# Performance work log

Hardware: AMD Instinct MI355X
Metric: run time of the kernel (lower is better)

The kernel has to match this reference:

```python
import jax, jax.numpy as jnp
import numpy as np

C = 3                     # num_classes
HNM_RATIO = 3
W_OBJ = W_CLS = W_LOC = 1.0
IOU_POS, IOU_NEG = 0.5, 0.4
B, M = 32, 16
SCALES = [(160, 160), (80, 80), (40, 40)]
SIZES = [0.08, 0.16, 0.28]     # A square anchor sizes per grid cell
A = len(SIZES)


def _grid_anchors(H, W):
    # anchors ordered as ((h*W + w)*A + a), matching the permute/reshape of predictions
    cy = (np.arange(H, dtype=np.float32) + 0.5) / H
    cx = (np.arange(W, dtype=np.float32) + 0.5) / W
    cyg, cxg = np.meshgrid(cy, cx, indexing='ij')                 # [H,W]
    cyg = np.broadcast_to(cyg[..., None], (H, W, A))
    cxg = np.broadcast_to(cxg[..., None], (H, W, A))
    sz = np.broadcast_to(np.asarray(SIZES, np.float32), (H, W, A))
    anc = np.stack([cxg, cyg, sz, sz], axis=-1).reshape(-1, 4)     # [H*W*A,4] cxcywh
    return jnp.asarray(anc)


def _corners(b):  # cxcywh -> x1y1x2y2
    return jnp.concatenate([b[..., :2] - b[..., 2:] / 2, b[..., :2] + b[..., 2:] / 2], axis=-1)


def _iou(a, b):  # a [N,4], b [M,4] in corner format -> [N,M]
    lt = jnp.maximum(a[:, None, :2], b[None, :, :2])
    rb = jnp.minimum(a[:, None, 2:], b[None, :, 2:])
    wh = jnp.clip(rb - lt, 0.0)
    inter = wh[..., 0] * wh[..., 1]
    aa = (a[:, 2] - a[:, 0]) * (a[:, 3] - a[:, 1])
    ab = (b[:, 2] - b[:, 0]) * (b[:, 3] - b[:, 1])
    return inter / (aa[:, None] + ab[None, :] - inter + 1e-9)


def _loss_one(P, boxes, labels, anc):
    # P: [A*(5+C), H, W]; boxes: [M,4] cxcywh; labels: [M] int; anc: [N,4] cxcywh
    Ch, H, Wd = P.shape
    N = H * Wd * A
    P = P.transpose(1, 2, 0).reshape(N, 5 + C)
    loc, obj, cls = P[:, :4], P[:, 4], P[:, 5:]
    # --- anchor matching ---
    iou = _iou(_corners(anc), _corners(boxes))            # [N,M]
    best = iou.max(axis=1)
    midx = iou.argmax(axis=1)
    pos = best >= IOU_POS
    neg = best < IOU_NEG
    mlab = labels[midx]                                   # [N]
    mbox = boxes[midx]                                    # [N,4]
    # --- objectness BCE with hard negative mining ---
    obj_t = pos.astype(obj.dtype)
    obj_all = jnp.maximum(obj, 0) - obj * obj_t + jnp.log1p(jnp.exp(-jnp.abs(obj)))
    obj_d = jax.lax.stop_gradient(obj_all)
    npos = pos.sum()
    avail = neg.sum()
    k = jnp.where(npos == 0, jnp.minimum(100, avail), jnp.minimum(HNM_RATIO * npos, avail))
    s = jnp.sort(jnp.where(neg, obj_d, -jnp.inf))[::-1]   # descending neg losses
    thr = s[jnp.clip(k - 1, 0, N - 1)]
    sel = jnp.where(k > 0, neg & (obj_d >= thr), neg)
    mask = pos | sel
    cnt = mask.sum()
    l_obj = jnp.where(cnt > 0, (obj_all * mask).sum() / jnp.maximum(cnt, 1), 0.0)
    # --- classification CE over positives ---
    logp = jax.nn.log_softmax(cls, axis=-1)
    cls_t = jnp.clip(mlab - 1, 0, C - 1)
    ce = -jnp.take_along_axis(logp, cls_t[:, None], axis=1)[:, 0]
    l_cls = jnp.where(npos > 0, (ce * pos).sum() / jnp.maximum(npos, 1), 0.0)
    # --- localization SmoothL1 over positives ---
    t = jnp.concatenate([(mbox[:, :2] - anc[:, :2]) / anc[:, 2:],
                         jnp.log(mbox[:, 2:] / anc[:, 2:])], axis=1)
    d = jnp.abs(loc - t)
    sl1 = jnp.where(d < 1.0, 0.5 * d * d, d - 0.5)
    l_loc = jnp.where(npos > 0, (sl1 * pos[:, None]).sum() / (jnp.maximum(npos, 1) * 4), 0.0)
    return l_obj, l_cls, l_loc


def setup_inputs() -> dict:
    key = jax.random.key(0)
    ks = jax.random.split(key, 7)
    preds = [jax.random.normal(ks[i], (B, A * (5 + C), H, W), dtype=jnp.float32)
             for i, (H, W) in enumerate(SCALES)]
    ancs = [_grid_anchors(H, W) for (H, W) in SCALES]
    cxy = jax.random.uniform(ks[3], (B, M, 2), minval=0.1, maxval=0.9)
    wh = jax.random.uniform(ks[4], (B, M, 2), minval=0.05, maxval=0.3)
    boxes = jnp.concatenate([cxy, wh], axis=-1).astype(jnp.float32)   # cxcywh
    labels = jax.random.randint(ks[5], (B, M), 1, C + 1, dtype=jnp.int32)
    return {"pred0": preds[0], "pred1": preds[1], "pred2": preds[2],
            "anc0": ancs[0], "anc1": ancs[1], "anc2": ancs[2],
            "boxes": boxes, "labels": labels}


def reference(pred0, pred1, pred2, anc0, anc1, anc2, boxes, labels):
    lo = lc = ll = 0.0
    for P, anc in ((pred0, anc0), (pred1, anc1), (pred2, anc2)):
        o, c, l = jax.vmap(_loss_one, in_axes=(0, 0, 0, None))(P, boxes, labels, anc)
        lo = lo + o.sum(); lc = lc + c.sum(); ll = ll + l.sum()
    Bn = pred0.shape[0]
    loss_obj, loss_cls, loss_loc = lo / Bn, lc / Bn, ll / Bn
    loss_total = W_OBJ * loss_obj + W_CLS * loss_cls + W_LOC * loss_loc
    return jnp.stack([loss_obj, loss_cls, loss_loc, loss_total])
```

## Files before the change

### kernel.cpp

```cpp
#include <hip/hip_runtime.h>
#include <math.h>

#define ANUM 3
#define CNUM 3
#define BNUM 32
#define MNUM 16
#define CH 24
#define NBIN 4096
#define NSEG 96
#define CAP 8192
#define CHUNK 4800
#define CPB 21

__device__ __align__(16) int   g_hist[NSEG*NBIN];
__device__ __align__(16) float g_cand[(size_t)NSEG*CAP];
__device__ int   g_ccnt[NSEG];
__device__ int   g_T[NSEG];
__device__ int   g_kk[NSEG];
__device__ int   g_cab[NSEG];
__device__ float g_sab[NSEG];
__device__ float g_acc[NSEG*5];
__device__ float g_lsum[3];
__device__ int   g_done;

__device__ __forceinline__ float wred(float v){
  #pragma unroll
  for (int off=32; off; off>>=1) v += __shfl_down(v, off, 64);
  return v;
}
__device__ __forceinline__ int wredi(int v){
  #pragma unroll
  for (int off=32; off; off>>=1) v += __shfl_down(v, off, 64);
  return v;
}

__device__ __forceinline__ void seg_map(int c, int& s, int& ci){
  if (c < 16){ s = 0; ci = c; }
  else if (c < 20){ s = 1; ci = c - 16; }
  else { s = 2; ci = 0; }
}
__device__ __forceinline__ void seg_geom(int s, int& N, size_t& segbase){
  N = (s==0) ? 76800 : ((s==1) ? 19200 : 4800);
  segbase = (s==0) ? 0
          : ((s==1) ? (size_t)BNUM*76800
                    : (size_t)BNUM*(76800+19200));
}

__global__ __launch_bounds__(256) void kinit(){
  const int gid = blockIdx.x*256 + threadIdx.x;
  ((int4*)g_hist)[gid] = make_int4(0,0,0,0);
  if (gid < NSEG*5) g_acc[gid] = 0.f;
  if (gid < 3) g_lsum[gid] = 0.f;
  if (gid == 3) g_done = 0;
  if (gid < NSEG){ g_ccnt[gid]=0; g_sab[gid]=0.f; }
}

template<int H, int W, int SCALE>
__device__ __forceinline__ void k1_work(
    const float* __restrict__ pred, float* __restrict__ negvals,
    const float* sbox, const int* slab, int b, int pix, int* lh, float* f)
{
  constexpr int HW = H*W;
  constexpr int N = HW*ANUM;
  constexpr size_t segbase = (SCALE==0) ? 0
                           : ((SCALE==1) ? (size_t)BNUM*76800
                                         : (size_t)BNUM*(76800+19200));
  const bool valid = (pix < HW);
  const int pp = valid ? pix : 0;
  const int h = pp / W, w = pp % W;
  const float cx = ((float)w + 0.5f)/(float)W;
  const float cy = ((float)h + 0.5f)/(float)H;

  const float* pb = pred + (size_t)b*CH*HW;
  float obj[3];
  #pragma unroll
  for (int a=0;a<3;a++) obj[a] = pb[(a*8+4)*HW + pp];

  float ax0[3],ay0[3],ax1[3],ay1[3],areaA[3];
  #pragma unroll
  for (int a=0;a<3;a++){
    const float sz=(a==0)?0.08f:((a==1)?0.16f:0.28f);
    const float hs=sz*0.5f;
    ax0[a]=cx-hs; ay0[a]=cy-hs; ax1[a]=cx+hs; ay1[a]=cy+hs;
    areaA[a]=(ax1[a]-ax0[a])*(ay1[a]-ay0[a]);
  }
  float bi[3]={-1.f,-1.f,-1.f}, bu[3]={1.f,1.f,1.f};
  int bm[3]={0,0,0};
  #pragma unroll
  for (int m=0;m<MNUM;m++){
    const float bcx=sbox[4*m], bcy=sbox[4*m+1], bw=sbox[4*m+2], bh=sbox[4*m+3];
    const float bx0=bcx-bw*0.5f, by0=bcy-bh*0.5f, bx1=bcx+bw*0.5f, by1=bcy+bh*0.5f;
    const float areaB=(bx1-bx0)*(by1-by0);
    #pragma unroll
    for (int a=0;a<3;a++){
      float iw=fminf(ax1[a],bx1)-fmaxf(ax0[a],bx0);
      float ih=fminf(ay1[a],by1)-fmaxf(ay0[a],by0);
      iw=fmaxf(iw,0.f); ih=fmaxf(ih,0.f);
      const float inter=iw*ih;
      const float uni=areaA[a]+areaB-inter+1e-9f;
      if (inter*bu[a] > bi[a]*uni){ bi[a]=inter; bu[a]=uni; bm[a]=m; }
    }
  }
  #pragma unroll
  for (int a=0;a<3;a++){
    const float best = bi[a]/bu[a];
    const bool pos = best >= 0.5f;
    const bool neg = best < 0.4f;
    const float o = obj[a];
    const float sp = log1pf(expf(-fabsf(o)));
    const float obj_all = fmaxf(o,0.f) - (pos? o:0.f) + sp;
    if (valid){
      negvals[segbase + (size_t)b*N + pp*3 + a] = neg ? obj_all : -1.f;
      if (neg){
        atomicAdd(&lh[__float_as_uint(obj_all)>>20], 1);
        f[1] += 1.f;
      }
      if (pos){
        f[0]+=1.f; f[2]+=obj_all;
        const int midx=bm[a];
        int ct = slab[midx]-1; ct = ct<0?0:(ct>CNUM-1?CNUM-1:ct);
        const int cb=a*8;
        float c0=pb[(cb+5)*HW+pp], c1=pb[(cb+6)*HW+pp], c2=pb[(cb+7)*HW+pp];
        float mx=fmaxf(c0,fmaxf(c1,c2));
        float lse=mx+logf(expf(c0-mx)+expf(c1-mx)+expf(c2-mx));
        float csel=(ct==0)?c0:((ct==1)?c1:c2);
        f[3]+=lse-csel;
        const float sz=(a==0)?0.08f:((a==1)?0.16f:0.28f);
        float mcx=sbox[4*midx],mcy=sbox[4*midx+1],mw=sbox[4*midx+2],mh=sbox[4*midx+3];
        float t0=(mcx-cx)/sz,t1=(mcy-cy)/sz,t2=logf(mw/sz),t3=logf(mh/sz);
        float l0=pb[(cb+0)*HW+pp],l1=pb[(cb+1)*HW+pp],l2=pb[(cb+2)*HW+pp],l3=pb[(cb+3)*HW+pp];
        float ssum=0.f,d;
        d=fabsf(l0-t0); ssum+=(d<1.f)?(0.5f*d*d):(d-0.5f);
        d=fabsf(l1-t1); ssum+=(d<1.f)?(0.5f*d*d):(d-0.5f);
        d=fabsf(l2-t2); ssum+=(d<1.f)?(0.5f*d*d):(d-0.5f);
        d=fabsf(l3-t3); ssum+=(d<1.f)?(0.5f*d*d):(d-0.5f);
        f[4]+=ssum;
      }
    }
  }
}

__global__ __launch_bounds__(256) void k1_all(
    const float* __restrict__ pred0, const float* __restrict__ pred1,
    const float* __restrict__ pred2, const float* __restrict__ boxes,
    const int* __restrict__ labels, float* __restrict__ negvals)
{
  __shared__ float sbox[MNUM*4];
  __shared__ int   slab[MNUM];
  __shared__ int   lh[NBIN];
  __shared__ float red[5][4];

  const int b = blockIdx.y;
  if (threadIdx.x < MNUM*4) sbox[threadIdx.x] = boxes[b*MNUM*4 + threadIdx.x];
  else if (threadIdx.x < MNUM*5) slab[threadIdx.x - MNUM*4] = labels[b*MNUM + (threadIdx.x - MNUM*4)];
  int4* lh4 = (int4*)lh;
  for (int i=threadIdx.x; i<NBIN/4; i+=256) lh4[i] = make_int4(0,0,0,0);
  __syncthreads();

  const int c = blockIdx.x;
  float f[5] = {0.f,0.f,0.f,0.f,0.f};
  int g;
  if (c < 100){ g = b;          k1_work<160,160,0>(pred0, negvals, sbox, slab, b, c*256 + (int)threadIdx.x, lh, f); }
  else if (c < 125){ g = BNUM + b; k1_work<80,80,1>(pred1, negvals, sbox, slab, b, (c-100)*256 + (int)threadIdx.x, lh, f); }
  else { g = 2*BNUM + b;        k1_work<40,40,2>(pred2, negvals, sbox, slab, b, (c-125)*256 + (int)threadIdx.x, lh, f); }

  const int lane = threadIdx.x & 63, wv = threadIdx.x >> 6;
  #pragma unroll
  for (int q=0;q<5;q++){
    float r = wred(f[q]);
    if (lane==0) red[q][wv] = r;
  }
  __syncthreads();
  if (threadIdx.x < 5){
    const int q = threadIdx.x;
    float t = red[q][0]+red[q][1]+red[q][2]+red[q][3];
    if (t != 0.f) atomicAdd(&g_acc[g*5+q], t);
  }
  int* gh = g_hist + (size_t)g*NBIN;
  for (int i=threadIdx.x; i<NBIN/4; i+=256){
    int4 hv = lh4[i];
    if (hv.x) atomicAdd(gh + i*4 + 0, hv.x);
    if (hv.y) atomicAdd(gh + i*4 + 1, hv.y);
    if (hv.z) atomicAdd(gh + i*4 + 2, hv.z);
    if (hv.w) atomicAdd(gh + i*4 + 3, hv.w);
  }
}

__global__ __launch_bounds__(256) void k2_pick(){
  const int g = blockIdx.x;
  const float* ag = g_acc + g*5;
  const float npos_f = ag[0], avail_f = ag[1];
  const int npos = (int)(npos_f + 0.5f);
  const int avail = (int)(avail_f + 0.5f);
  const int k = (npos==0) ? (avail < 100 ? avail : 100)
                          : (3*npos < avail ? 3*npos : avail);
  const int* hist = g_hist + (size_t)g*NBIN;

  __shared__ int tsum[256];
  __shared__ int s_tt, s_cum;

  const int4* h4 = (const int4*)(hist + threadIdx.x*16);
  int ssum = 0;
  #pragma unroll
  for (int i=0;i<4;i++){ int4 v = h4[i]; ssum += v.x+v.y+v.z+v.w; }
  tsum[threadIdx.x] = ssum;
  __syncthreads();

  if (k > 0){
    if (threadIdx.x==0){
      int cum=0, tt=0;
      for (int t=255;t>=0;t--){
        if (cum + tsum[t] >= k){ tt=t; break; }
        cum += tsum[t];
      }
      s_tt = tt; s_cum = cum;
    }
    __syncthreads();
    if (threadIdx.x == s_tt){
      int cum = s_cum, T=0, kk=0;
      for (int j=15;j>=0;j--){
        int c = hist[s_tt*16 + j];
        if (cum + c >= k){ T = s_tt*16 + j; kk = k - cum; break; }
        cum += c;
      }
      g_T[g]=T; g_kk[g]=kk; g_cab[g]=cum;
    }
  } else if (threadIdx.x==0){
    g_T[g]=0x7FFFFFFF; g_kk[g]=0; g_cab[g]=0;
  }
}

__global__ __launch_bounds__(256) void k2_scan(const float* __restrict__ negvals){
  const int bid = blockIdx.x;
  const int b = bid / CPB;
  int s, ci; seg_map(bid % CPB, s, ci);
  const int g = s*BNUM + b;
  int N; size_t segbase; seg_geom(s, N, segbase);
  const float* seg = negvals + segbase + (size_t)b*N + (size_t)ci*CHUNK;
  const int T = g_T[g];
  const int lane = threadIdx.x & 63;

  const float4* p4 = (const float4*)seg;
  float sab = 0.f; int cnt = 0;

  for (int i = threadIdx.x; i < CHUNK/4; i += 256){
    float4 v4 = p4[i];
    #pragma unroll
    for (int j=0;j<4;j++){
      float v = (&v4.x)[j];
      if (v < 0.f) continue;
      const int bin = (int)(__float_as_uint(v) >> 20);
      if (bin > T) sab += v;
      else if (bin == T) cnt++;
    }
  }

  __shared__ float redf[4];
  __shared__ int   redi[4];
  __shared__ int   s_base, s_loc;
  float r = wred(sab); int c = wredi(cnt);
  if (lane == 0){ redf[threadIdx.x>>6] = r; redi[threadIdx.x>>6] = c; }
  __syncthreads();
  if (threadIdx.x == 0){
    float t = redf[0]+redf[1]+redf[2]+redf[3];
    int   n = redi[0]+redi[1]+redi[2]+redi[3];
    if (t != 0.f) atomicAdd(&g_sab[g], t);
    s_base = (n > 0) ? atomicAdd(&g_ccnt[g], n) : 0;
    s_loc = 0;
  }
  __syncthreads();
  const int base = s_base;

  if (__syncthreads_count(cnt > 0) == 0) return;
  for (int i = threadIdx.x; i < CHUNK/4; i += 256){
    float4 v4 = p4[i];
    #pragma unroll
    for (int j=0;j<4;j++){
      float v = (&v4.x)[j];
      const bool isT = (v >= 0.f) && ((int)(__float_as_uint(v) >> 20) == T);
      unsigned long long peers = __ballot(isT ? 1 : 0);
      if (isT){
        const int leader = __ffsll(peers) - 1;
        int wbase = 0;
        if (lane == leader) wbase = atomicAdd(&s_loc, (int)__popcll(peers));
        wbase = __shfl(wbase, leader, 64);
        const int idx = base + wbase + (int)__popcll(peers & ((1ull<<lane)-1ull));
        if (idx < CAP) g_cand[(size_t)g*CAP + idx] = v;
      }
    }
  }
}

__global__ __launch_bounds__(256) void k2_fin(const float* __restrict__ negvals, float* __restrict__ out){
  const int g = blockIdx.x;
  const int s = g >> 5;
  const int b = g & 31;
  int N; size_t segbase; seg_geom(s, N, segbase);
  const float* seg = negvals + segbase + (size_t)b*N;

  const float* ag = g_acc + g*5;
  const float npos_f = ag[0], avail_f = ag[1];
  const int npos = (int)(npos_f + 0.5f);
  const int avail = (int)(avail_f + 0.5f);
  const int k = (npos==0) ? (avail < 100 ? avail : 100)
                          : (3*npos < avail ? 3*npos : avail);

  __shared__ float cv[CAP];
  __shared__ int hist[256];
  __shared__ int s_bin, s_rem;
  __shared__ float red[2][4];

  float ss = 0.f, ns = 0.f;
  float sab = 0.f, cab_f = 0.f;

  if (k > 0){
    const int T = g_T[g];
    const int kk0 = g_kk[g];
    const int cab = g_cab[g];
    sab = g_sab[g];
    cab_f = (float)cab;
    const int C = g_ccnt[g];

    unsigned prel = 0, pm = 0;
    int rem = kk0;

    if (C <= CAP){
      for (int i=threadIdx.x; i<C; i+=256) cv[i] = g_cand[(size_t)g*CAP + i];
      __syncthreads();
      #pragma unroll
      for (int p=0;p<3;p++){
        const int shift = (p==0)?12:((p==1)?4:0);
        const unsigned bmax = (p==2)?15u:255u;
        hist[threadIdx.x] = 0;
        __syncthreads();
        for (int i=threadIdx.x; i<C; i+=256){
          unsigned u20 = __float_as_uint(cv[i]) & 0xFFFFFu;
          if ((u20 & pm) == prel) atomicAdd(&hist[(u20>>shift)&bmax], 1);
        }
        __syncthreads();
        if (threadIdx.x==0){
          int cum=0;
          for (int j=(int)bmax;j>=0;j--){
            cum += hist[j];
            if (cum >= rem){ s_bin=j; s_rem = rem-(cum-hist[j]); break; }
          }
        }
        __syncthreads();
        prel |= ((unsigned)s_bin << shift);
        pm |= (bmax << shift);
        rem = s_rem;
        __syncthreads();
      }
      const float thr = __uint_as_float(((unsigned)T << 20) | prel);
      for (int i=threadIdx.x; i<C; i+=256){
        float v = cv[i];
        if (v >= thr){ ss += v; ns += 1.f; }
      }
    } else {
      const float4* p4 = (const float4*)seg;
      const int N4 = N >> 2;
      #pragma unroll
      for (int p=0;p<3;p++){
        const int shift = (p==0)?12:((p==1)?4:0);
        const unsigned bmax = (p==2)?15u:255u;
        hist[threadIdx.x] = 0;
        __syncthreads();
        for (int i=threadIdx.x; i<N4; i+=256){
          float4 v4 = p4[i];
          #pragma unroll
          for (int j=0;j<4;j++){
            float v = (&v4.x)[j];
            if (v < 0.f) continue;
            unsigned u = __float_as_uint(v);
            if ((int)(u >> 20) != T) continue;
            unsigned u20 = u & 0xFFFFFu;
            if ((u20 & pm) == prel) atomicAdd(&hist[(u20>>shift)&bmax], 1);
          }
        }
        __syncthreads();
        if (threadIdx.x==0){
          int cum=0;
          for (int j=(int)bmax;j>=0;j--){
            cum += hist[j];
            if (cum >= rem){ s_bin=j; s_rem = rem-(cum-hist[j]); break; }
          }
        }
        __syncthreads();
        prel |= ((unsigned)s_bin << shift);
        pm |= (bmax << shift);
        rem = s_rem;
        __syncthreads();
      }
      const float thr = __uint_as_float(((unsigned)T << 20) | prel);
      for (int i=threadIdx.x; i<N4; i+=256){
        float4 v4 = p4[i];
        #pragma unroll
        for (int j=0;j<4;j++){
          float v = (&v4.x)[j];
          if (v < 0.f) continue;
          if ((int)(__float_as_uint(v) >> 20) == T && v >= thr){ ss += v; ns += 1.f; }
        }
      }
    }
  }

  const int lane = threadIdx.x & 63, wv = threadIdx.x >> 6;
  float r0 = wred(ss), r1 = wred(ns);
  if (lane==0){ red[0][wv]=r0; red[1][wv]=r1; }
  __syncthreads();
  if (threadIdx.x==0){
    float sstot = sab + red[0][0]+red[0][1]+red[0][2]+red[0][3];
    float nstot = cab_f + red[1][0]+red[1][1]+red[1][2]+red[1][3];
    float cnt = npos_f + nstot;
    float lo = (cnt > 0.f) ? (ag[2] + sstot)/cnt : 0.f;
    float lc = (npos > 0) ? ag[3]/npos_f : 0.f;
    float ll = (npos > 0) ? ag[4]/(npos_f*4.f) : 0.f;
    atomicAdd(&g_lsum[0], lo);
    atomicAdd(&g_lsum[1], lc);
    atomicAdd(&g_lsum[2], ll);
    __threadfence();
    if (atomicAdd(&g_done, 1) == NSEG-1){
      float L0 = atomicAdd(&g_lsum[0], 0.f);
      float L1 = atomicAdd(&g_lsum[1], 0.f);
      float L2 = atomicAdd(&g_lsum[2], 0.f);
      float lo2 = L0*(1.f/32.f), lc2 = L1*(1.f/32.f), ll2 = L2*(1.f/32.f);
      out[0]=lo2; out[1]=lc2; out[2]=ll2; out[3]=lo2+lc2+ll2;
    }
  }
}

extern "C" void kernel_launch(void* const* d_in, const int* in_sizes, int n_in,
                              void* d_out, int out_size, void* d_ws, size_t ws_size,
                              hipStream_t stream)
{
  const float* pred0 = (const float*)d_in[0];
  const float* pred1 = (const float*)d_in[1];
  const float* pred2 = (const float*)d_in[2];
  const float* boxes = (const float*)d_in[6];
  const int*   labels = (const int*)d_in[7];
  float* out = (float*)d_out;

  float* negvals = (float*)d_ws;

  kinit<<<384, 256, 0, stream>>>();
  k1_all<<<dim3(132,32), 256, 0, stream>>>(pred0, pred1, pred2, boxes, labels, negvals);
  k2_pick<<<96, 256, 0, stream>>>();
  k2_scan<<<672, 256, 0, stream>>>(negvals);
  k2_fin<<<96, 256, 0, stream>>>(negvals, out);
}
```

Measured before the change: 232.1 us.

## Fuse pick into k1 and fin into scan using last-block atomic counters

Removes two kernel launches by having the last block per segment in k1_all compute the threshold-bin pick, and the last block per segment in the scan kernel do the final top-k refinement and loss reduction. Completion is detected with per-segment arrival counters using acquire-release atomics, and shared cross-block data is read through agent-scope atomic loads. This cuts launch and inter-kernel gap overhead. In exchange, the scan kernel now reserves a large shared candidate buffer in every block, which may lower occupancy, and the tail work is serialized onto the last-arriving block.

```diff
diff --git a/kernel.cpp b/kernel.cpp
--- a/kernel.cpp
+++ b/kernel.cpp
@@ -21,6 +21,8 @@
 __device__ float g_sab[NSEG];
 __device__ float g_acc[NSEG*5];
 __device__ float g_lsum[3];
+__device__ int   g_arr1[NSEG];
+__device__ int   g_arr2[NSEG];
 __device__ int   g_done;
 
 __device__ __forceinline__ float wred(float v){
@@ -52,7 +54,7 @@
   if (gid < NSEG*5) g_acc[gid] = 0.f;
   if (gid < 3) g_lsum[gid] = 0.f;
   if (gid == 3) g_done = 0;
-  if (gid < NSEG){ g_ccnt[gid]=0; g_sab[gid]=0.f; }
+  if (gid < NSEG){ g_ccnt[gid]=0; g_sab[gid]=0.f; g_arr1[gid]=0; g_arr2[gid]=0; }
 }
 
 template<int H, int W, int SCALE>
@@ -159,10 +161,13 @@
 
   const int c = blockIdx.x;
   float f[5] = {0.f,0.f,0.f,0.f,0.f};
-  int g;
-  if (c < 100){ g = b;          k1_work<160,160,0>(pred0, negvals, sbox, slab, b, c*256 + (int)threadIdx.x, lh, f); }
-  else if (c < 125){ g = BNUM + b; k1_work<80,80,1>(pred1, negvals, sbox, slab, b, (c-100)*256 + (int)threadIdx.x, lh, f); }
-  else { g = 2*BNUM + b;        k1_work<40,40,2>(pred2, negvals, sbox, slab, b, (c-125)*256 + (int)threadIdx.x, lh, f); }
+  int g, nblk;
+  if (c < 100){ g = b; nblk = 100;
+    k1_work<160,160,0>(pred0, negvals, sbox, slab, b, c*256 + (int)threadIdx.x, lh, f); }
+  else if (c < 125){ g = BNUM + b; nblk = 25;
+    k1_work<80,80,1>(pred1, negvals, sbox, slab, b, (c-100)*256 + (int)threadIdx.x, lh, f); }
+  else { g = 2*BNUM + b; nblk = 7;
+    k1_work<40,40,2>(pred2, negvals, sbox, slab, b, (c-125)*256 + (int)threadIdx.x, lh, f); }
 
   const int lane = threadIdx.x & 63, wv = threadIdx.x >> 6;
   #pragma unroll
@@ -184,26 +189,36 @@
     if (hv.z) atomicAdd(gh + i*4 + 2, hv.z);
     if (hv.w) atomicAdd(gh + i*4 + 3, hv.w);
   }
-}
-
-__global__ __launch_bounds__(256) void k2_pick(){
-  const int g = blockIdx.x;
-  const float* ag = g_acc + g*5;
-  const float npos_f = ag[0], avail_f = ag[1];
-  const int npos = (int)(npos_f + 0.5f);
-  const int avail = (int)(avail_f + 0.5f);
+  __syncthreads();
+
+  __shared__ int s_lastb;
+  if (threadIdx.x==0){
+    int prev = __hip_atomic_fetch_add(&g_arr1[g], 1, __ATOMIC_ACQ_REL, __HIP_MEMORY_SCOPE_AGENT);
+    s_lastb = (prev == nblk-1) ? 1 : 0;
+  }
+  __syncthreads();
+  if (!s_lastb) return;
+
+  for (int i=threadIdx.x; i<NBIN; i+=256)
+    lh[i] = __hip_atomic_load(gh + i, __ATOMIC_RELAXED, __HIP_MEMORY_SCOPE_AGENT);
+  __shared__ float s_np, s_av;
+  if (threadIdx.x==0){
+    s_np = __hip_atomic_load(&g_acc[g*5+0], __ATOMIC_RELAXED, __HIP_MEMORY_SCOPE_AGENT);
+    s_av = __hip_atomic_load(&g_acc[g*5+1], __ATOMIC_RELAXED, __HIP_MEMORY_SCOPE_AGENT);
+  }
+  __syncthreads();
+
+  const int npos = (int)(s_np + 0.5f);
+  const int avail = (int)(s_av + 0.5f);
   const int k = (npos==0) ? (avail < 100 ? avail : 100)
                           : (3*npos < avail ? 3*npos : avail);
-  const int* hist = g_hist + (size_t)g*NBIN;
 
   __shared__ int tsum[256];
   __shared__ int s_tt, s_cum;
-
-  const int4* h4 = (const int4*)(hist + threadIdx.x*16);
-  int ssum = 0;
-  #pragma unroll
-  for (int i=0;i<4;i++){ int4 v = h4[i]; ssum += v.x+v.y+v.z+v.w; }
-  tsum[threadIdx.x] = ssum;
+  int ssum2 = 0;
+  #pragma unroll
+  for (int i=0;i<16;i++) ssum2 += lh[threadIdx.x*16 + i];
+  tsum[threadIdx.x] = ssum2;
   __syncthreads();
 
   if (k > 0){
@@ -219,9 +234,9 @@
     if (threadIdx.x == s_tt){
       int cum = s_cum, T=0, kk=0;
       for (int j=15;j>=0;j--){
-        int c = hist[s_tt*16 + j];
-        if (cum + c >= k){ T = s_tt*16 + j; kk = k - cum; break; }
-        cum += c;
+        int cc = lh[s_tt*16 + j];
+        if (cum + cc >= k){ T = s_tt*16 + j; kk = k - cum; break; }
+        cum += cc;
       }
       g_T[g]=T; g_kk[g]=kk; g_cab[g]=cum;
     }
@@ -230,17 +245,28 @@
   }
 }
 
-__global__ __launch_bounds__(256) void k2_scan(const float* __restrict__ negvals){
+__global__ __launch_bounds__(256) void k2_scanfin(
+    const float* __restrict__ negvals, float* __restrict__ out)
+{
   const int bid = blockIdx.x;
   const int b = bid / CPB;
   int s, ci; seg_map(bid % CPB, s, ci);
   const int g = s*BNUM + b;
   int N; size_t segbase; seg_geom(s, N, segbase);
-  const float* seg = negvals + segbase + (size_t)b*N + (size_t)ci*CHUNK;
+  const float* segc = negvals + segbase + (size_t)b*N + (size_t)ci*CHUNK;
   const int T = g_T[g];
   const int lane = threadIdx.x & 63;
-
-  const float4* p4 = (const float4*)seg;
+  const int nblk = (s==0) ? 16 : ((s==1) ? 4 : 1);
+
+  __shared__ float cv[CAP];
+  __shared__ int hist[256];
+  __shared__ int s_bin, s_rem, s_lastb;
+  __shared__ float redf[4];
+  __shared__ int   redi[4];
+  __shared__ int   s_base, s_loc;
+  __shared__ float red2[2][4];
+
+  const float4* p4 = (const float4*)segc;
   float sab = 0.f; int cnt = 0;
 
   for (int i = threadIdx.x; i < CHUNK/4; i += 256){
@@ -255,11 +281,8 @@
     }
   }
 
-  __shared__ float redf[4];
-  __shared__ int   redi[4];
-  __shared__ int   s_base, s_loc;
-  float r = wred(sab); int c = wredi(cnt);
-  if (lane == 0){ redf[threadIdx.x>>6] = r; redi[threadIdx.x>>6] = c; }
+  float r = wred(sab); int c2 = wredi(cnt);
+  if (lane == 0){ redf[threadIdx.x>>6] = r; redi[threadIdx.x>>6] = c2; }
   __syncthreads();
   if (threadIdx.x == 0){
     float t = redf[0]+redf[1]+redf[2]+redf[3];
@@ -270,62 +293,72 @@
   }
   __syncthreads();
   const int base = s_base;
-
-  if (__syncthreads_count(cnt > 0) == 0) return;
-  for (int i = threadIdx.x; i < CHUNK/4; i += 256){
-    float4 v4 = p4[i];
-    #pragma unroll
-    for (int j=0;j<4;j++){
-      float v = (&v4.x)[j];
-      const bool isT = (v >= 0.f) && ((int)(__float_as_uint(v) >> 20) == T);
-      unsigned long long peers = __ballot(isT ? 1 : 0);
-      if (isT){
-        const int leader = __ffsll(peers) - 1;
-        int wbase = 0;
-        if (lane == leader) wbase = atomicAdd(&s_loc, (int)__popcll(peers));
-        wbase = __shfl(wbase, leader, 64);
-        const int idx = base + wbase + (int)__popcll(peers & ((1ull<<lane)-1ull));
-        if (idx < CAP) g_cand[(size_t)g*CAP + idx] = v;
-      }
-    }
-  }
-}
-
-__global__ __launch_bounds__(256) void k2_fin(const float* __restrict__ negvals, float* __restrict__ out){
-  const int g = blockIdx.x;
-  const int s = g >> 5;
-  const int b = g & 31;
-  int N; size_t segbase; seg_geom(s, N, segbase);
+  const bool anyT = (__syncthreads_count(cnt > 0) != 0);
+
+  if (anyT){
+    for (int i = threadIdx.x; i < CHUNK/4; i += 256){
+      float4 v4 = p4[i];
+      #pragma unroll
+      for (int j=0;j<4;j++){
+        float v = (&v4.x)[j];
+        const bool isT = (v >= 0.f) && ((int)(__float_as_uint(v) >> 20) == T);
+        unsigned long long peers = __ballot(isT ? 1 : 0);
+        if (isT){
+          const int leader = __ffsll(peers) - 1;
+          int wbase = 0;
+          if (lane == leader) wbase = atomicAdd(&s_loc, (int)__popcll(peers));
+          wbase = __shfl(wbase, leader, 64);
+          const int idx = base + wbase + (int)__popcll(peers & ((1ull<<lane)-1ull));
+          if (idx < CAP)
+            __hip_atomic_store(&g_cand[(size_t)g*CAP + idx], v,
+                               __ATOMIC_RELAXED, __HIP_MEMORY_SCOPE_AGENT);
+        }
+      }
+    }
+  }
+  __syncthreads();
+
+  if (threadIdx.x==0){
+    int prev = __hip_atomic_fetch_add(&g_arr2[g], 1, __ATOMIC_ACQ_REL, __HIP_MEMORY_SCOPE_AGENT);
+    s_lastb = (prev == nblk-1) ? 1 : 0;
+  }
+  __syncthreads();
+  if (!s_lastb) return;
+
   const float* seg = negvals + segbase + (size_t)b*N;
-
-  const float* ag = g_acc + g*5;
-  const float npos_f = ag[0], avail_f = ag[1];
+  __shared__ float s_np, s_av, s_sab;
+  __shared__ int s_C;
+  if (threadIdx.x==0){
+    s_np  = __hip_atomic_load(&g_acc[g*5+0], __ATOMIC_RELAXED, __HIP_MEMORY_SCOPE_AGENT);
+    s_av  = __hip_atomic_load(&g_acc[g*5+1], __ATOMIC_RELAXED, __HIP_MEMORY_SCOPE_AGENT);
+    s_sab = __hip_atomic_load(&g_sab[g],     __ATOMIC_RELAXED, __HIP_MEMORY_SCOPE_AGENT);
+    s_C   = __hip_atomic_load(&g_ccnt[g],    __ATOMIC_RELAXED, __HIP_MEMORY_SCOPE_AGENT);
+  }
+  __syncthreads();
+
+  const float npos_f = s_np;
   const int npos = (int)(npos_f + 0.5f);
-  const int avail = (int)(avail_f + 0.5f);
+  const int avail = (int)(s_av + 0.5f);
   const int k = (npos==0) ? (avail < 100 ? avail : 100)
                           : (3*npos < avail ? 3*npos : avail);
 
-  __shared__ float cv[CAP];
-  __shared__ int hist[256];
-  __shared__ int s_bin, s_rem;
-  __shared__ float red[2][4];
-
   float ss = 0.f, ns = 0.f;
-  float sab = 0.f, cab_f = 0.f;
+  float sab2 = 0.f, cab_f = 0.f;
 
   if (k > 0){
-    const int T = g_T[g];
     const int kk0 = g_kk[g];
     const int cab = g_cab[g];
-    sab = g_sab[g];
+    sab2 = s_sab;
     cab_f = (float)cab;
-    const int C = g_ccnt[g];
+    const int C = s_C;
 
     unsigned prel = 0, pm = 0;
     int rem = kk0;
 
     if (C <= CAP){
-      for (int i=threadIdx.x; i<C; i+=256) cv[i] = g_cand[(size_t)g*CAP + i];
+      for (int i=threadIdx.x; i<C; i+=256)
+        cv[i] = __hip_atomic_load(&g_cand[(size_t)g*CAP + i],
+                                  __ATOMIC_RELAXED, __HIP_MEMORY_SCOPE_AGENT);
       __syncthreads();
       #pragma unroll
       for (int p=0;p<3;p++){
@@ -357,7 +390,7 @@
         if (v >= thr){ ss += v; ns += 1.f; }
       }
     } else {
-      const float4* p4 = (const float4*)seg;
+      const float4* q4 = (const float4*)seg;
       const int N4 = N >> 2;
       #pragma unroll
       for (int p=0;p<3;p++){
@@ -366,7 +399,7 @@
         hist[threadIdx.x] = 0;
         __syncthreads();
         for (int i=threadIdx.x; i<N4; i+=256){
-          float4 v4 = p4[i];
+          float4 v4 = q4[i];
           #pragma unroll
           for (int j=0;j<4;j++){
             float v = (&v4.x)[j];
@@ -393,7 +426,7 @@
       }
       const float thr = __uint_as_float(((unsigned)T << 20) | prel);
       for (int i=threadIdx.x; i<N4; i+=256){
-        float4 v4 = p4[i];
+        float4 v4 = q4[i];
         #pragma unroll
         for (int j=0;j<4;j++){
           float v = (&v4.x)[j];
@@ -404,25 +437,28 @@
     }
   }
 
-  const int lane = threadIdx.x & 63, wv = threadIdx.x >> 6;
+  const int wv = threadIdx.x >> 6;
   float r0 = wred(ss), r1 = wred(ns);
-  if (lane==0){ red[0][wv]=r0; red[1][wv]=r1; }
+  if (lane==0){ red2[0][wv]=r0; red2[1][wv]=r1; }
   __syncthreads();
   if (threadIdx.x==0){
-    float sstot = sab + red[0][0]+red[0][1]+red[0][2]+red[0][3];
-    float nstot = cab_f + red[1][0]+red[1][1]+red[1][2]+red[1][3];
-    float cnt = npos_f + nstot;
-    float lo = (cnt > 0.f) ? (ag[2] + sstot)/cnt : 0.f;
-    float lc = (npos > 0) ? ag[3]/npos_f : 0.f;
-    float ll = (npos > 0) ? ag[4]/(npos_f*4.f) : 0.f;
+    float sstot = sab2 + red2[0][0]+red2[0][1]+red2[0][2]+red2[0][3];
+    float nstot = cab_f + red2[1][0]+red2[1][1]+red2[1][2]+red2[1][3];
+    float cnt2 = npos_f + nstot;
+    float ag2 = __hip_atomic_load(&g_acc[g*5+2], __ATOMIC_RELAXED, __HIP_MEMORY_SCOPE_AGENT);
+    float ag3 = __hip_atomic_load(&g_acc[g*5+3], __ATOMIC_RELAXED, __HIP_MEMORY_SCOPE_AGENT);
+    float ag4 = __hip_atomic_load(&g_acc[g*5+4], __ATOMIC_RELAXED, __HIP_MEMORY_SCOPE_AGENT);
+    float lo = (cnt2 > 0.f) ? (ag2 + sstot)/cnt2 : 0.f;
+    float lc = (npos > 0) ? ag3/npos_f : 0.f;
+    float ll = (npos > 0) ? ag4/(npos_f*4.f) : 0.f;
     atomicAdd(&g_lsum[0], lo);
     atomicAdd(&g_lsum[1], lc);
     atomicAdd(&g_lsum[2], ll);
     __threadfence();
-    if (atomicAdd(&g_done, 1) == NSEG-1){
-      float L0 = atomicAdd(&g_lsum[0], 0.f);
-      float L1 = atomicAdd(&g_lsum[1], 0.f);
-      float L2 = atomicAdd(&g_lsum[2], 0.f);
+    if (__hip_atomic_fetch_add(&g_done, 1, __ATOMIC_ACQ_REL, __HIP_MEMORY_SCOPE_AGENT) == NSEG-1){
+      float L0 = __hip_atomic_load(&g_lsum[0], __ATOMIC_RELAXED, __HIP_MEMORY_SCOPE_AGENT);
+      float L1 = __hip_atomic_load(&g_lsum[1], __ATOMIC_RELAXED, __HIP_MEMORY_SCOPE_AGENT);
+      float L2 = __hip_atomic_load(&g_lsum[2], __ATOMIC_RELAXED, __HIP_MEMORY_SCOPE_AGENT);
       float lo2 = L0*(1.f/32.f), lc2 = L1*(1.f/32.f), ll2 = L2*(1.f/32.f);
       out[0]=lo2; out[1]=lc2; out[2]=ll2; out[3]=lo2+lc2+ll2;
     }
@@ -444,7 +480,5 @@
 
   kinit<<<384, 256, 0, stream>>>();
   k1_all<<<dim3(132,32), 256, 0, stream>>>(pred0, pred1, pred2, boxes, labels, negvals);
-  k2_pick<<<96, 256, 0, stream>>>();
-  k2_scan<<<672, 256, 0, stream>>>(negvals);
-  k2_fin<<<96, 256, 0, stream>>>(negvals, out);
-}
+  k2_scanfin<<<672, 256, 0, stream>>>(negvals, out);
+}
```

After: 377.5 us. +62.7%, slower.
